# Kernel tuning notes

Measured on AMD Instinct MI355X. Metric: run time of the kernel, lower is better.

Reference implementation:

```python
import jax, jax.numpy as jnp
import numpy as np

NEG = -1e30  # finite stand-in for -inf (keeps grads NaN-free)

T, B, V, L = 1024, 64, 128, 256


def setup_inputs() -> dict:
    key = jax.random.key(0)
    k1, k2 = jax.random.split(key)
    acts = jax.random.normal(k1, (T, B, V), dtype=jnp.float32)
    # flat concatenated labels, values in [1, V) (0 is the blank)
    labels = jax.random.randint(k2, (B * L,), 1, V, dtype=jnp.int32)
    act_lens = jnp.full((B,), T, dtype=jnp.int32)
    label_lens = jnp.full((B,), L, dtype=jnp.int32)
    return {"acts": acts, "labels": labels, "act_lens": act_lens, "label_lens": label_lens}


def _ctc_costs(acts, labels, act_lens, label_lens):
    # warp-ctc takes raw activations and applies softmax internally
    Tt, Bb, Vv = acts.shape
    Ll = labels.shape[0] // Bb
    blank = 0
    lab = labels.reshape(Bb, Ll)
    S = 2 * Ll + 1
    # extended label seq: blank, l1, blank, l2, ..., blank  -> (B, S)
    ext = jnp.full((Bb, S), blank, dtype=labels.dtype).at[:, 1::2].set(lab)
    # skip transition allowed where ext[s] != blank and ext[s] != ext[s-2]
    allow = jnp.concatenate(
        [jnp.zeros((Bb, 2), dtype=bool), (ext[:, 2:] != blank) & (ext[:, 2:] != ext[:, :-2])],
        axis=1,
    )
    log_probs = jax.nn.log_softmax(acts, axis=-1)  # (T, B, V)
    # emission log-probs along the extended label sequence: (T, B, S)
    emit_all = jnp.take_along_axis(log_probs, jnp.broadcast_to(ext[None], (Tt, Bb, S)), axis=2)

    alpha0 = (
        jnp.full((Bb, S), NEG, dtype=acts.dtype)
        .at[:, 0].set(emit_all[0, :, 0])
        .at[:, 1].set(emit_all[0, :, 1])
    )

    def step(alpha, xs):
        emit, t = xs  # emit: (B, S)
        p1 = jnp.pad(alpha[:, :-1], ((0, 0), (1, 0)), constant_values=NEG)
        p2 = jnp.pad(alpha[:, :-2], ((0, 0), (2, 0)), constant_values=NEG)
        p2 = jnp.where(allow, p2, NEG)
        m = jnp.maximum(jnp.maximum(alpha, p1), p2)
        new = m + jnp.log(jnp.exp(alpha - m) + jnp.exp(p1 - m) + jnp.exp(p2 - m)) + emit
        # freeze rows whose act_len is exhausted
        alpha = jnp.where((t < act_lens)[:, None], new, alpha)
        return alpha, None

    alphaT, _ = jax.lax.scan(step, alpha0, (emit_all[1:], jnp.arange(1, Tt)))
    end = (2 * label_lens).astype(jnp.int32)  # last blank position per example
    a_end = jnp.take_along_axis(alphaT, end[:, None], axis=1)[:, 0]
    a_end1 = jnp.take_along_axis(alphaT, (end - 1)[:, None], axis=1)[:, 0]
    return -jnp.logaddexp(a_end, a_end1)  # per-example negative log-likelihood


def reference(acts, labels, act_lens, label_lens):
    costs = _ctc_costs(acts, labels, act_lens, label_lens)
    return jnp.sum(costs)  # reduce=True, no size/length averaging
```

## Files before the change

### kernel.cpp

```cpp
#include <hip/hip_runtime.h>
#include <hip/hip_fp16.h>
#include <math.h>


#define L2E 1.4426950408889634f
#define LN2 0.6931471805599453f

constexpr int T   = 1024;
constexpr int B   = 64;
constexpr int V   = 128;
constexpr int L   = 256;
constexpr int RW  = 256;
constexpr int TP  = T + 32;

typedef float v2f __attribute__((ext_vector_type(2)));
typedef unsigned int v2u __attribute__((ext_vector_type(2)));

__device__ __forceinline__ v2f pk_add(v2f a, v2f b) {
  v2f d; asm("v_pk_add_f32 %0, %1, %2" : "=v"(d) : "v"(a), "v"(b)); return d;
}
__device__ __forceinline__ v2f pk_mul(v2f a, v2f b) {
  v2f d; asm("v_pk_mul_f32 %0, %1, %2" : "=v"(d) : "v"(a), "v"(b)); return d;
}
__device__ __forceinline__ v2f pk_fma(v2f a, v2f b, v2f c) {
  v2f d; asm("v_pk_fma_f32 %0, %1, %2, %3" : "=v"(d) : "v"(a), "v"(b), "v"(c));
  return d;
}

template <int CTRL>
__device__ __forceinline__ float fdpp0(float x) {
  return __int_as_float(__builtin_amdgcn_update_dpp(
      0, __float_as_int(x), CTRL, 0xf, 0xf, true));
}
template <int CTRL>
__device__ __forceinline__ float fdppk(float x) {
  return __int_as_float(__builtin_amdgcn_update_dpp(
      __float_as_int(x), __float_as_int(x), CTRL, 0xf, 0xf, false));
}

__device__ __forceinline__ float wave_bcast63(float x) {
  return __int_as_float(__builtin_amdgcn_readlane(__float_as_int(x), 63));
}

__device__ __forceinline__ float wave_max(float x) {
  x = fmaxf(x, fdppk<0x111>(x));
  x = fmaxf(x, fdppk<0x112>(x));
  x = fmaxf(x, fdppk<0x114>(x));
  x = fmaxf(x, fdppk<0x118>(x));
  x = fmaxf(x, fdppk<0x142>(x));
  x = fmaxf(x, fdppk<0x143>(x));
  return wave_bcast63(x);
}
__device__ __forceinline__ float wave_sum_nn(float x) {
  x += fdpp0<0x111>(x);
  x += fdpp0<0x112>(x);
  x += fdpp0<0x114>(x);
  x += fdpp0<0x118>(x);
  x += fdpp0<0x142>(x);
  x += fdpp0<0x143>(x);
  return wave_bcast63(x);
}

__device__ __forceinline__ float h2f(uint bits) {
  return __half2float(__ushort_as_half((ushort)bits));
}

__global__ __launch_bounds__(512) void ctc_probs_kernel(
    const float* __restrict__ acts,
    const int* __restrict__ labels,
    ushort* __restrict__ P,
    float* __restrict__ Pbk) {
  const int w    = threadIdx.x >> 6;
  const int lane = threadIdx.x & 63;
  const int t    = blockIdx.x * 8 + w;
  const int b    = blockIdx.y;
  ushort* prow = P + ((size_t)b * TP + t) * RW;

  if (t >= T) {
    uint2 z; z.x = 0u; z.y = 0u;
    *(uint2*)(prow + 4 * lane) = z;
    if (lane == 0) {
      v2f zp; zp.x = 0.f; zp.y = 0.f;
      *(v2f*)(Pbk + ((size_t)b * TP + t) * 2) = zp;
    }
    return;
  }

  const float* row = acts + ((size_t)t * B + b) * V;
  const float2 v2 = *(const float2*)(row + 2 * lane);
  const float e0 = exp2f(fmaf(v2.x, L2E, -32.0f));
  const float e1 = exp2f(fmaf(v2.y, L2E, -32.0f));
  const float sm = wave_sum_nn(e0 + e1);
  const float r  = __builtin_amdgcn_rcpf(sm);

  const auto pk = __builtin_amdgcn_cvt_pkrtz(e0 * r, e1 * r);
  uint hp;
  __builtin_memcpy(&hp, &pk, 4);

  const int4 lv = *(const int4*)(labels + (size_t)b * L + 4 * lane);
  const uint g0 = (uint)__builtin_amdgcn_ds_bpermute((lv.x & ~1) * 2, (int)hp);
  const uint g1 = (uint)__builtin_amdgcn_ds_bpermute((lv.y & ~1) * 2, (int)hp);
  const uint g2 = (uint)__builtin_amdgcn_ds_bpermute((lv.z & ~1) * 2, (int)hp);
  const uint g3 = (uint)__builtin_amdgcn_ds_bpermute((lv.w & ~1) * 2, (int)hp);
  const uint h0 = (g0 >> ((lv.x & 1) << 4)) & 0xffffu;
  const uint h1 = (g1 >> ((lv.y & 1) << 4)) & 0xffffu;
  const uint h2 = (g2 >> ((lv.z & 1) << 4));
  const uint h3 = (g3 >> ((lv.w & 1) << 4));
  uint2 o;
  o.x = h0 | (h2 << 16);
  o.y = h1 | (h3 << 16);
  *(uint2*)(prow + 4 * lane) = o;
  if (lane == 0) {
    const float pb = e0 * r;
    v2f bp; bp.x = pb; bp.y = pb;
    *(v2f*)(Pbk + ((size_t)b * TP + t) * 2) = bp;
  }
}

__global__ __launch_bounds__(64) void ctc_dp_kernel(
    const ushort* __restrict__ P,
    const float* __restrict__ Pbk,
    const int* __restrict__ labels,
    const int* __restrict__ act_lens,
    const int* __restrict__ label_lens,
    float* __restrict__ out) {
  const int b    = blockIdx.x;
  const int lane = threadIdx.x;
  const ushort* __restrict__ Pb = P + (size_t)b * TP * RW;
  const float*  __restrict__ Bk = Pbk + (size_t)b * TP * 2;

  const int4 lv   = *(const int4*)(labels + (size_t)b * L + 4 * lane);
  const int prevw = __builtin_amdgcn_update_dpp(0, lv.w, 0x138, 0xf, 0xf, true);
  const float f0 = (lane > 0 && lv.x != 0 && lv.x != prevw) ? 1.f : 0.f;
  const float f1 = (lv.y != 0 && lv.y != lv.x) ? 1.f : 0.f;
  const float f2 = (lv.z != 0 && lv.z != lv.y) ? 1.f : 0.f;
  const float f3 = (lv.w != 0 && lv.w != lv.z) ? 1.f : 0.f;
  v2f F02; F02.x = f0; F02.y = f2;
  v2f F13; F13.x = f1; F13.y = f3;

  const int AL = act_lens[b];

  v2f P0, P1, P2, P3;
  P0.x=0.f; P0.y=0.f; P1.x=0.f; P1.y=0.f;
  P2.x=0.f; P2.y=0.f; P3.x=0.f; P3.y=0.f;
  float a8 = 0.f;
  {
    const uint2 u0 = *(const uint2*)(Pb + 4 * lane);
    const v2f bk0  = *(const v2f*)(Bk);
    const float eb0 = bk0.x;
    const float e00 = h2f(u0.x);
    if (lane == 0) { P0.x = eb0; P1.x = e00; }
  }
  int iacc = 0;
  float pend = 1.0f;

  auto step = [&](v2u u, v2f eb) {
    const float pc = fdpp0<0x138>(P3.y);
    v2f Q; Q.x = pc; Q.y = P3.x;
    v2f E02, E13;
    E02.x = h2f(u.x); E02.y = h2f(u.x >> 16);
    E13.x = h2f(u.y); E13.y = h2f(u.y >> 16);
    const float s8 = a8 + P3.y;
    const v2f S3 = pk_add(P3, P2);
    const v2f T3 = pk_fma(F13, P1, S3);
    const v2f S2 = pk_add(P2, P1);
    const v2f S1 = pk_add(P1, P0);
    const v2f S0 = pk_add(P0, Q);
    const v2f T1 = pk_fma(F02, Q,  S1);
    P3 = pk_mul(T3, E13);
    P2 = pk_mul(S2, eb);
    P1 = pk_mul(T1, E02);
    P0 = pk_mul(S0, eb);
    a8 = s8 * eb.x;
  };

  auto measure = [&]() {
    float m = fmaxf(fmaxf(fmaxf(P0.x, P0.y), fmaxf(P1.x, P1.y)),
                    fmaxf(fmaxf(P2.x, P2.y), fmaxf(P3.x, P3.y)));
    m = fmaxf(m, a8);
    pend = wave_max(m);
  };
  auto apply = [&]() {
    const uint mb = __float_as_uint(pend);
    int e = (int)((mb >> 23) & 0xffu); if (e < 48) e = 48;
    const float r = __uint_as_float((uint)(302 - e) << 23);
    iacc += (e - 175);
    v2f rr; rr.x = r; rr.y = r;
    P0 = pk_mul(P0, rr); P1 = pk_mul(P1, rr);
    P2 = pk_mul(P2, rr); P3 = pk_mul(P3, rr);
    a8 *= r;
  };

  uint2 evi[16];
  v2f   ebk[16];
  #pragma unroll
  for (int k = 0; k < 16; ++k) {
    evi[k] = *(const uint2*)(Pb + (size_t)(1 + k) * RW + 4 * lane);
    ebk[k] = *(const v2f*)(Bk + (size_t)(1 + k) * 2);
  }

  const ushort* pf = Pb + (size_t)17 * RW;
  const float*  bf = Bk + (size_t)17 * 2;
  int t0 = 1;
  #pragma unroll 1
  for (int blk = 0; blk < 64; ++blk) {
    const ushort* pfA = pf;
    const ushort* pfB = pf + (size_t)8 * RW;
    const bool fast = (t0 + 16 <= AL);
    if (fast) {
      #pragma unroll
      for (int k = 0; k < 16; ++k) {
        const uint2 uu = evi[k];
        v2u u; u.x = uu.x; u.y = uu.y;
        const v2f  eb = ebk[k];
        evi[k] = *(const uint2*)(((k < 8) ? pfA : pfB)
                                 + (size_t)(k & 7) * RW + 4 * lane);
        ebk[k] = *(const v2f*)(bf + (size_t)k * 2);
        step(u, eb);
        if (k == 13) measure();
        if (k == 15) apply();
      }
    } else {
      #pragma unroll
      for (int k = 0; k < 16; ++k) {
        const uint2 uu = evi[k];
        v2u u; u.x = uu.x; u.y = uu.y;
        const v2f  eb = ebk[k];
        evi[k] = *(const uint2*)(((k < 8) ? pfA : pfB)
                                 + (size_t)(k & 7) * RW + 4 * lane);
        ebk[k] = *(const v2f*)(bf + (size_t)k * 2);
        if ((t0 + k) < AL) step(u, eb);
        if (k == 13) measure();
        if (k == 15) apply();
      }
    }
    t0 += 16;
    pf += (size_t)16 * RW;
    bf += (size_t)16 * 2;
  }

  const int end  = 2 * label_lens[b];
  const int base = 8 * lane;
  float sel = 0.f;
  if (base     == end || base     == end - 1) sel += P0.x;
  if (base + 1 == end || base + 1 == end - 1) sel += P1.x;
  if (base + 2 == end || base + 2 == end - 1) sel += P2.x;
  if (base + 3 == end || base + 3 == end - 1) sel += P3.x;
  if (base + 4 == end || base + 4 == end - 1) sel += P0.y;
  if (base + 5 == end || base + 5 == end - 1) sel += P1.y;
  if (base + 6 == end || base + 6 == end - 1) sel += P2.y;
  if (base + 7 == end || base + 7 == end - 1) sel += P3.y;
  if (lane == 63 && (end == 512 || end - 1 == 512)) sel += a8;
  sel = wave_sum_nn(sel);
  if (lane == 0) {
    const float cost = -((log2f(sel) + (float)iacc) * LN2);
    atomicAdd(out, cost);
  }
}

extern "C" void kernel_launch(void* const* d_in, const int* in_sizes, int n_in,
                              void* d_out, int out_size, void* d_ws, size_t ws_size,
                              hipStream_t stream) {
  const float* acts       = (const float*)d_in[0];
  const int*   labels     = (const int*)d_in[1];
  const int*   act_lens   = (const int*)d_in[2];
  const int*   label_lens = (const int*)d_in[3];
  float* out = (float*)d_out;
  ushort* P   = (ushort*)d_ws;
  float*  Pbk = (float*)(P + (size_t)B * TP * RW);

  (void)hipMemsetAsync(out, 0, sizeof(float) * out_size, stream);
  ctc_probs_kernel<<<dim3(TP / 8, B), 512, 0, stream>>>(acts, labels, P, Pbk);
  ctc_dp_kernel<<<B, 64, 0, stream>>>(P, Pbk, labels, act_lens, label_lens, out);
}
```

Measured before the change: 146.6 us.

## Restructure CTC DP step with scalar blank operands and batch probs rows per wave

The probs kernel now has each wave handle eight timesteps, so the label loads and bpermute address math are amortised across rows. The DP step is rewritten so each state update ends in an FMA, and the blank probability is passed as an SGPR operand. Blank-prob values for the next 16-step block are loaded up front as uniform loads. The aim is a shorter serial dependency chain per step and fewer vector registers and loads on the latency-bound recurrence, at the cost of slightly different rounding.

```diff
diff --git a/kernel.cpp b/kernel.cpp
--- a/kernel.cpp
+++ b/kernel.cpp
@@ -16,14 +16,18 @@
 typedef float v2f __attribute__((ext_vector_type(2)));
 typedef unsigned int v2u __attribute__((ext_vector_type(2)));
 
-__device__ __forceinline__ v2f pk_add(v2f a, v2f b) {
-  v2f d; asm("v_pk_add_f32 %0, %1, %2" : "=v"(d) : "v"(a), "v"(b)); return d;
+__device__ __forceinline__ v2f pk_fma(v2f a, v2f b, v2f c) {
+  v2f d; asm("v_pk_fma_f32 %0, %1, %2, %3" : "=v"(d) : "v"(a), "v"(b), "v"(c));
+  return d;
 }
 __device__ __forceinline__ v2f pk_mul(v2f a, v2f b) {
   v2f d; asm("v_pk_mul_f32 %0, %1, %2" : "=v"(d) : "v"(a), "v"(b)); return d;
 }
-__device__ __forceinline__ v2f pk_fma(v2f a, v2f b, v2f c) {
-  v2f d; asm("v_pk_fma_f32 %0, %1, %2, %3" : "=v"(d) : "v"(a), "v"(b), "v"(c));
+__device__ __forceinline__ v2f pk_mul_s(v2f a, v2f sb) {
+  v2f d; asm("v_pk_mul_f32 %0, %1, %2" : "=v"(d) : "v"(a), "s"(sb)); return d;
+}
+__device__ __forceinline__ v2f pk_fma_s(v2f a, v2f sb, v2f c) {
+  v2f d; asm("v_pk_fma_f32 %0, %1, %2, %3" : "=v"(d) : "v"(a), "s"(sb), "v"(c));
   return d;
 }
 
@@ -65,55 +69,64 @@
   return __half2float(__ushort_as_half((ushort)bits));
 }
 
-__global__ __launch_bounds__(512) void ctc_probs_kernel(
+__global__ __launch_bounds__(256) void ctc_probs_kernel(
     const float* __restrict__ acts,
     const int* __restrict__ labels,
     ushort* __restrict__ P,
     float* __restrict__ Pbk) {
   const int w    = threadIdx.x >> 6;
   const int lane = threadIdx.x & 63;
-  const int t    = blockIdx.x * 8 + w;
   const int b    = blockIdx.y;
-  ushort* prow = P + ((size_t)b * TP + t) * RW;
-
-  if (t >= T) {
-    uint2 z; z.x = 0u; z.y = 0u;
-    *(uint2*)(prow + 4 * lane) = z;
+  const int tb   = blockIdx.x * 32 + w * 8;
+
+  if (tb >= T) {
+    #pragma unroll
+    for (int r = 0; r < 8; ++r) {
+      uint2 z; z.x = 0u; z.y = 0u;
+      *(uint2*)(P + ((size_t)b * TP + tb + r) * RW + 4 * lane) = z;
+    }
+    if (lane < 8) {
+      v2f zp; zp.x = 0.f; zp.y = 0.f;
+      *(v2f*)(Pbk + ((size_t)b * TP + tb + lane) * 2) = zp;
+    }
+    return;
+  }
+
+  const int4 lvv = *(const int4*)(labels + (size_t)b * L + 4 * lane);
+  const int ba0 = (lvv.x & ~1) * 2, sh0 = (lvv.x & 1) << 4;
+  const int ba1 = (lvv.y & ~1) * 2, sh1 = (lvv.y & 1) << 4;
+  const int ba2 = (lvv.z & ~1) * 2, sh2 = (lvv.z & 1) << 4;
+  const int ba3 = (lvv.w & ~1) * 2, sh3 = (lvv.w & 1) << 4;
+
+  #pragma unroll
+  for (int r = 0; r < 8; ++r) {
+    const int t = tb + r;
+    const float* row = acts + ((size_t)t * B + b) * V;
+    const float2 v2 = *(const float2*)(row + 2 * lane);
+    const float e0 = exp2f(fmaf(v2.x, L2E, -32.0f));
+    const float e1 = exp2f(fmaf(v2.y, L2E, -32.0f));
+    const float sm = wave_sum_nn(e0 + e1);
+    const float rc = __builtin_amdgcn_rcpf(sm);
+    const auto pk = __builtin_amdgcn_cvt_pkrtz(e0 * rc, e1 * rc);
+    uint hp;
+    __builtin_memcpy(&hp, &pk, 4);
+    const uint g0 = (uint)__builtin_amdgcn_ds_bpermute(ba0, (int)hp);
+    const uint g1 = (uint)__builtin_amdgcn_ds_bpermute(ba1, (int)hp);
+    const uint g2 = (uint)__builtin_amdgcn_ds_bpermute(ba2, (int)hp);
+    const uint g3 = (uint)__builtin_amdgcn_ds_bpermute(ba3, (int)hp);
+    const uint h0 = (g0 >> sh0) & 0xffffu;
+    const uint h1 = (g1 >> sh1) & 0xffffu;
+    const uint h2 = (g2 >> sh2);
+    const uint h3 = (g3 >> sh3);
+    uint2 o;
+    o.x = h0 | (h2 << 16);
+    o.y = h1 | (h3 << 16);
+    *(uint2*)(P + ((size_t)b * TP + t) * RW + 4 * lane) = o;
     if (lane == 0) {
-      v2f zp; zp.x = 0.f; zp.y = 0.f;
-      *(v2f*)(Pbk + ((size_t)b * TP + t) * 2) = zp;
-    }
-    return;
-  }
-
-  const float* row = acts + ((size_t)t * B + b) * V;
-  const float2 v2 = *(const float2*)(row + 2 * lane);
-  const float e0 = exp2f(fmaf(v2.x, L2E, -32.0f));
-  const float e1 = exp2f(fmaf(v2.y, L2E, -32.0f));
-  const float sm = wave_sum_nn(e0 + e1);
-  const float r  = __builtin_amdgcn_rcpf(sm);
-
-  const auto pk = __builtin_amdgcn_cvt_pkrtz(e0 * r, e1 * r);
-  uint hp;
-  __builtin_memcpy(&hp, &pk, 4);
-
-  const int4 lv = *(const int4*)(labels + (size_t)b * L + 4 * lane);
-  const uint g0 = (uint)__builtin_amdgcn_ds_bpermute((lv.x & ~1) * 2, (int)hp);
-  const uint g1 = (uint)__builtin_amdgcn_ds_bpermute((lv.y & ~1) * 2, (int)hp);
-  const uint g2 = (uint)__builtin_amdgcn_ds_bpermute((lv.z & ~1) * 2, (int)hp);
-  const uint g3 = (uint)__builtin_amdgcn_ds_bpermute((lv.w & ~1) * 2, (int)hp);
-  const uint h0 = (g0 >> ((lv.x & 1) << 4)) & 0xffffu;
-  const uint h1 = (g1 >> ((lv.y & 1) << 4)) & 0xffffu;
-  const uint h2 = (g2 >> ((lv.z & 1) << 4));
-  const uint h3 = (g3 >> ((lv.w & 1) << 4));
-  uint2 o;
-  o.x = h0 | (h2 << 16);
-  o.y = h1 | (h3 << 16);
-  *(uint2*)(prow + 4 * lane) = o;
-  if (lane == 0) {
-    const float pb = e0 * r;
-    v2f bp; bp.x = pb; bp.y = pb;
-    *(v2f*)(Pbk + ((size_t)b * TP + t) * 2) = bp;
+      const float pb = e0 * rc;
+      v2f bp; bp.x = pb; bp.y = pb;
+      *(v2f*)(Pbk + ((size_t)b * TP + t) * 2) = bp;
+    }
   }
 }
 
@@ -160,18 +173,18 @@
     v2f E02, E13;
     E02.x = h2f(u.x); E02.y = h2f(u.x >> 16);
     E13.x = h2f(u.y); E13.y = h2f(u.y >> 16);
-    const float s8 = a8 + P3.y;
-    const v2f S3 = pk_add(P3, P2);
-    const v2f T3 = pk_fma(F13, P1, S3);
-    const v2f S2 = pk_add(P2, P1);
-    const v2f S1 = pk_add(P1, P0);
-    const v2f S0 = pk_add(P0, Q);
-    const v2f T1 = pk_fma(F02, Q,  S1);
-    P3 = pk_mul(T3, E13);
-    P2 = pk_mul(S2, eb);
-    P1 = pk_mul(T1, E02);
-    P0 = pk_mul(S0, eb);
-    a8 = s8 * eb.x;
+    const v2f A1 = pk_fma(F02, Q, P0);
+    const v2f A3 = pk_fma(F13, P1, P2);
+    const v2f ZQ = pk_mul_s(Q, eb);
+    const v2f Z2 = pk_mul_s(P1, eb);
+    const v2f Z1 = pk_mul(A1, E02);
+    const v2f Z3 = pk_mul(A3, E13);
+    const float z8 = P3.y * eb.x;
+    P0 = pk_fma_s(P0, eb, ZQ);
+    P1 = pk_fma(P1, E02, Z1);
+    P2 = pk_fma_s(P2, eb, Z2);
+    P3 = pk_fma(P3, E13, Z3);
+    a8 = fmaf(a8, eb.x, z8);
   };
 
   auto measure = [&]() {
@@ -192,18 +205,24 @@
   };
 
   uint2 evi[16];
-  v2f   ebk[16];
   #pragma unroll
-  for (int k = 0; k < 16; ++k) {
+  for (int k = 0; k < 16; ++k)
     evi[k] = *(const uint2*)(Pb + (size_t)(1 + k) * RW + 4 * lane);
-    ebk[k] = *(const v2f*)(Bk + (size_t)(1 + k) * 2);
-  }
+  v2f ebq[16];
+  #pragma unroll
+  for (int k = 0; k < 16; ++k)
+    ebq[k] = *(const v2f*)(Bk + (size_t)(1 + k) * 2);
 
   const ushort* pf = Pb + (size_t)17 * RW;
-  const float*  bf = Bk + (size_t)17 * 2;
   int t0 = 1;
   #pragma unroll 1
   for (int blk = 0; blk < 64; ++blk) {
+    v2f ebn[16];
+    {
+      const float* bn = Bk + (size_t)(t0 + 16) * 2;
+      #pragma unroll
+      for (int k = 0; k < 16; ++k) ebn[k] = *(const v2f*)(bn + 2 * k);
+    }
     const ushort* pfA = pf;
     const ushort* pfB = pf + (size_t)8 * RW;
     const bool fast = (t0 + 16 <= AL);
@@ -212,11 +231,9 @@
       for (int k = 0; k < 16; ++k) {
         const uint2 uu = evi[k];
         v2u u; u.x = uu.x; u.y = uu.y;
-        const v2f  eb = ebk[k];
         evi[k] = *(const uint2*)(((k < 8) ? pfA : pfB)
                                  + (size_t)(k & 7) * RW + 4 * lane);
-        ebk[k] = *(const v2f*)(bf + (size_t)k * 2);
-        step(u, eb);
+        step(u, ebq[k]);
         if (k == 13) measure();
         if (k == 15) apply();
       }
@@ -225,18 +242,17 @@
       for (int k = 0; k < 16; ++k) {
         const uint2 uu = evi[k];
         v2u u; u.x = uu.x; u.y = uu.y;
-        const v2f  eb = ebk[k];
         evi[k] = *(const uint2*)(((k < 8) ? pfA : pfB)
                                  + (size_t)(k & 7) * RW + 4 * lane);
-        ebk[k] = *(const v2f*)(bf + (size_t)k * 2);
-        if ((t0 + k) < AL) step(u, eb);
+        if ((t0 + k) < AL) step(u, ebq[k]);
         if (k == 13) measure();
         if (k == 15) apply();
       }
     }
+    #pragma unroll
+    for (int k = 0; k < 16; ++k) ebq[k] = ebn[k];
     t0 += 16;
     pf += (size_t)16 * RW;
-    bf += (size_t)16 * 2;
   }
 
   const int end  = 2 * label_lens[b];
@@ -270,6 +286,6 @@
   float*  Pbk = (float*)(P + (size_t)B * TP * RW);
 
   (void)hipMemsetAsync(out, 0, sizeof(float) * out_size, stream);
-  ctc_probs_kernel<<<dim3(TP / 8, B), 512, 0, stream>>>(acts, labels, P, Pbk);
+  ctc_probs_kernel<<<dim3(TP / 32, B), 256, 0, stream>>>(acts, labels, P, Pbk);
   ctc_dp_kernel<<<B, 64, 0, stream>>>(P, Pbk, labels, act_lens, label_lens, out);
 }
```

Measured after the change: 150.2 us. 2.4% more time.
